# Kernel optimization log

Measured on AMD Instinct MI355X. Metric: run time of the kernel, lower is better.

Reference implementation:

```python
import jax, jax.numpy as jnp
import numpy as np
import math

SIZE = 11
PAD = 5
C1 = 0.01 ** 2
C2 = 0.03 ** 2


def gaussian_window():
    # Matches torch __init__: 1D gaussian (sigma=1.5), normalized, outer product,
    # expanded to depthwise weight of shape (3, 1, 11, 11)
    x = np.arange(SIZE, dtype=np.float32)
    g = np.exp(-((x - SIZE // 2) ** 2) / (2.0 * 1.5 ** 2)).astype(np.float32)
    g = g / g.sum()
    w2d = np.outer(g, g).astype(np.float32)  # (11, 11)
    return jnp.asarray(np.broadcast_to(w2d, (3, 1, SIZE, SIZE)).copy())


def depthwise_conv(x, win):
    return jax.lax.conv_general_dilated(
        x, win,
        window_strides=(1, 1),
        padding=[(PAD, PAD), (PAD, PAD)],
        dimension_numbers=('NCHW', 'OIHW', 'NCHW'),
        feature_group_count=3,
    )


def setup_inputs() -> dict:
    key = jax.random.key(0)
    k1, k2 = jax.random.split(key)
    img1 = jax.random.uniform(k1, (16, 3, 512, 512), dtype=jnp.float32)
    img2 = jax.random.uniform(k2, (16, 3, 512, 512), dtype=jnp.float32)
    return {"img1": img1, "img2": img2, "win": gaussian_window()}


def reference(img1, img2, win):
    mu1 = depthwise_conv(img1, win)
    mu2 = depthwise_conv(img2, win)
    mu1_sq = mu1 * mu1
    mu2_sq = mu2 * mu2
    mu1_mu2 = mu1 * mu2
    sig1_sq = depthwise_conv(img1 * img1, win) - mu1_sq
    sig2_sq = depthwise_conv(img2 * img2, win) - mu2_sq
    sig12 = depthwise_conv(img1 * img2, win) - mu1_mu2
    v = ((2.0 * mu1_mu2 + C1) * (2.0 * sig12 + C2)) / (
        (mu1_sq + mu2_sq + C1) * (sig1_sq + sig2_sq + C2))
    return 1.0 - jnp.mean(v)
```

## Files before the change

### kernel.cpp

```cpp
#include <hip/hip_runtime.h>


#define IMG 512
#define NPIX (16LL * 3 * 512 * 512)
#define GX 8
#define GY 16
#define NBLK (GX * GY * 48)
#define NPART NBLK

typedef short v8s __attribute__((ext_vector_type(8)));
typedef float v4f __attribute__((ext_vector_type(4)));
typedef __bf16 bf2 __attribute__((ext_vector_type(2)));
typedef float f2  __attribute__((ext_vector_type(2)));

static __device__ __forceinline__ int cvtpk2(f2 v) {
    bf2 r = __builtin_convertvector(v, bf2);
    return __builtin_bit_cast(int, r);
}
static __device__ __forceinline__ unsigned f2bf(float f) {
    unsigned u = __float_as_uint(f);
    return (u + 0x7FFFu + ((u >> 16) & 1u)) >> 16;
}

template <bool EDGE>
static __device__ __forceinline__ void load_rt(
    const float* __restrict__ p1, const float* __restrict__ p2,
    int grow, int gcol,
    float4& a0, float4& a1, float4& b0, float4& b1)
{
    if (!EDGE) {
        const float* r1 = p1 + (size_t)grow * IMG + gcol;
        const float* r2 = p2 + (size_t)grow * IMG + gcol;
        a0 = *(const float4*)r1;       a1 = *(const float4*)(r1 + 4);
        b0 = *(const float4*)r2;       b1 = *(const float4*)(r2 + 4);
    } else {
        float4 z4; z4.x = z4.y = z4.z = z4.w = 0.f;
        a0 = a1 = b0 = b1 = z4;
        if ((unsigned)grow < IMG) {
            const float* r1 = p1 + (size_t)grow * IMG;
            const float* r2 = p2 + (size_t)grow * IMG;
            if ((unsigned)gcol < IMG) {
                a0 = *(const float4*)(r1 + gcol);
                b0 = *(const float4*)(r2 + gcol);
            }
            if ((unsigned)(gcol + 4) < IMG) {
                a1 = *(const float4*)(r1 + gcol + 4);
                b1 = *(const float4*)(r2 + gcol + 4);
            }
        }
    }
}

static __device__ __forceinline__ void h_rt(
    float4 a0, float4 a1, float4 b0, float4 b1,
    v8s band, short (*hw)[16][40], int lm, int quad, int slot)
{
    const v4f zacc = {0.f, 0.f, 0.f, 0.f};
    f2 a0l; a0l.x = a0.x; a0l.y = a0.y;   f2 a0h; a0h.x = a0.z; a0h.y = a0.w;
    f2 a1l; a1l.x = a1.x; a1l.y = a1.y;   f2 a1h; a1h.x = a1.z; a1h.y = a1.w;
    f2 b0l; b0l.x = b0.x; b0l.y = b0.y;   f2 b0h; b0h.x = b0.z; b0h.y = b0.w;
    f2 b1l; b1l.x = b1.x; b1l.y = b1.y;   f2 b1h; b1h.x = b1.z; b1h.y = b1.w;

    v8s A[4]; int4 w;
    w.x = cvtpk2(a0l); w.y = cvtpk2(a0h); w.z = cvtpk2(a1l); w.w = cvtpk2(a1h);
    A[0] = __builtin_bit_cast(v8s, w);
    w.x = cvtpk2(b0l); w.y = cvtpk2(b0h); w.z = cvtpk2(b1l); w.w = cvtpk2(b1h);
    A[1] = __builtin_bit_cast(v8s, w);
    w.x = cvtpk2(__builtin_elementwise_fma(a0l, a0l, b0l * b0l));
    w.y = cvtpk2(__builtin_elementwise_fma(a0h, a0h, b0h * b0h));
    w.z = cvtpk2(__builtin_elementwise_fma(a1l, a1l, b1l * b1l));
    w.w = cvtpk2(__builtin_elementwise_fma(a1h, a1h, b1h * b1h));
    A[2] = __builtin_bit_cast(v8s, w);
    w.x = cvtpk2(a0l * b0l); w.y = cvtpk2(a0h * b0h);
    w.z = cvtpk2(a1l * b1l); w.w = cvtpk2(a1h * b1h);
    A[3] = __builtin_bit_cast(v8s, w);

    #pragma unroll
    for (int p = 0; p < 4; ++p) {
        const v4f acc = __builtin_amdgcn_mfma_f32_16x16x32_bf16(A[p], band, zacc, 0, 0, 0);
        int2 w2;
        f2 lo; lo.x = acc[0]; lo.y = acc[1];
        f2 hi; hi.x = acc[2]; hi.y = acc[3];
        w2.x = cvtpk2(lo); w2.y = cvtpk2(hi);
        *(int2*)&hw[p][lm][slot * 16 + quad * 4] = w2;
    }
}

static __device__ __forceinline__ void v_t2(
    v8s band, short (*hw)[16][40], int lm, int quad, int t2, f2& vsum)
{
    const v4f zacc = {0.f, 0.f, 0.f, 0.f};
    const int bs = (quad * 8 + t2 * 16) & 31;
    v4f acc[4];
    #pragma unroll
    for (int p = 0; p < 4; ++p) {
        const v8s hf = *(const v8s*)&hw[p][lm][bs];
        acc[p] = __builtin_amdgcn_mfma_f32_16x16x32_bf16(band, hf, zacc, 0, 0, 0);
    }
    const f2 C1v = {1e-4f, 1e-4f};
    const f2 C2v = {9e-4f, 9e-4f};
    const f2 two = {2.f, 2.f};
    #pragma unroll
    for (int h = 0; h < 2; ++h) {
        f2 m1; m1.x = acc[0][2 * h]; m1.y = acc[0][2 * h + 1];
        f2 m2; m2.x = acc[1][2 * h]; m2.y = acc[1][2 * h + 1];
        f2 es; es.x = acc[2][2 * h]; es.y = acc[2][2 * h + 1];
        f2 ex; ex.x = acc[3][2 * h]; ex.y = acc[3][2 * h + 1];
        const f2 m1s = m1 * m1, m2s = m2 * m2, m12 = m1 * m2;
        const f2 sig = es - m1s - m2s;
        const f2 s12 = ex - m12;
        const f2 num = __builtin_elementwise_fma(two, m12, C1v) *
                       __builtin_elementwise_fma(two, s12, C2v);
        const f2 den = (m1s + m2s + C1v) * (sig + C2v);
        f2 r; r.x = __builtin_amdgcn_rcpf(den.x); r.y = __builtin_amdgcn_rcpf(den.y);
        vsum = __builtin_elementwise_fma(num, r, vsum);
    }
}

__global__ __launch_bounds__(256, 6) void ssim_kernel(
    const float* __restrict__ img1,
    const float* __restrict__ img2,
    const float* __restrict__ win,
    float* __restrict__ partial)
{
    __shared__ __align__(16) short hb[4][4][16][40];

    const int tid  = threadIdx.x;
    const int lane = tid & 63;
    const int wave = tid >> 6;
    const int lm   = lane & 15;
    const int quad = lane >> 4;

    const int bx = blockIdx.x, by = blockIdx.y, z = blockIdx.z;
    const int ty0 = by * 32;

    float gl = 0.f;
    if (lane < 11) gl = win[55 + lane] * rsqrtf(win[60]);
    v8s band;
    #pragma unroll
    for (int j = 0; j < 8; ++j) {
        const int t  = quad * 8 + j - lm - 3;
        const int tc = ((unsigned)t > 10u) ? 11 : t;
        band[j] = (short)f2bf(__shfl(gl, tc));
    }

    const size_t zoff = (size_t)z * IMG * IMG;
    const float* p1 = img1 + zoff;
    const float* p2 = img2 + zoff;

    const int gct = bx * 4 + wave;
    const bool interior = (by > 0) & (by < GY - 1) & (gct > 0) & (gct < 31);
    const int gcol = gct * 16 - 8 + quad * 8;
    short (*hw)[16][40] = hb[wave];

    f2 vsum = {0.f, 0.f};
    {
        float4 a0[2], b0[2], a1[2], b1[2], a2[2], b2[2];
        if (interior) {
            load_rt<false>(p1, p2, ty0 - 8 + 0 * 16 + lm, gcol, a0[0], a0[1], b0[0], b0[1]);
            load_rt<false>(p1, p2, ty0 - 8 + 1 * 16 + lm, gcol, a1[0], a1[1], b1[0], b1[1]);
        } else {
            load_rt<true >(p1, p2, ty0 - 8 + 0 * 16 + lm, gcol, a0[0], a0[1], b0[0], b0[1]);
            load_rt<true >(p1, p2, ty0 - 8 + 1 * 16 + lm, gcol, a1[0], a1[1], b1[0], b1[1]);
        }
        h_rt(a0[0], a0[1], b0[0], b0[1], band, hw, lm, quad, 0);
        h_rt(a1[0], a1[1], b1[0], b1[1], band, hw, lm, quad, 1);
        if (interior)
            load_rt<false>(p1, p2, ty0 - 8 + 2 * 16 + lm, gcol, a2[0], a2[1], b2[0], b2[1]);
        else
            load_rt<true >(p1, p2, ty0 - 8 + 2 * 16 + lm, gcol, a2[0], a2[1], b2[0], b2[1]);
        v_t2(band, hw, lm, quad, 0, vsum);
        h_rt(a2[0], a2[1], b2[0], b2[1], band, hw, lm, quad, 0);
        v_t2(band, hw, lm, quad, 1, vsum);
    }

    float vs = vsum.x + vsum.y;
    #pragma unroll
    for (int off = 32; off > 0; off >>= 1)
        vs += __shfl_down(vs, off, 64);
    if (lane == 0) *(float*)&hb[wave][3][15][36] = vs;
    __syncthreads();
    if (tid == 0) {
        float t = 0.f;
        #pragma unroll
        for (int w = 0; w < 4; ++w) t += *(const float*)&hb[w][3][15][36];
        partial[(z * GY + by) * GX + bx] = t;
    }
}

__global__ __launch_bounds__(512) void finalize_kernel(
    const float* __restrict__ partial, float* __restrict__ out)
{
    __shared__ float red[8];
    const float4* p4 = (const float4*)partial;
    float s = 0.f;
    #pragma unroll
    for (int i = 0; i < NPART / 4 / 512; ++i) {
        const float4 t = p4[i * 512 + threadIdx.x];
        s += (t.x + t.y) + (t.z + t.w);
    }
    #pragma unroll
    for (int off = 32; off > 0; off >>= 1)
        s += __shfl_down(s, off, 64);
    if ((threadIdx.x & 63) == 0) red[threadIdx.x >> 6] = s;
    __syncthreads();
    if (threadIdx.x == 0) {
        float t = 0.f;
        #pragma unroll
        for (int i = 0; i < 8; ++i) t += red[i];
        out[0] = 1.0f - t / (float)NPIX;
    }
}

extern "C" void kernel_launch(void* const* d_in, const int* in_sizes, int n_in,
                              void* d_out, int out_size, void* d_ws, size_t ws_size,
                              hipStream_t stream) {
    const float* img1 = (const float*)d_in[0];
    const float* img2 = (const float*)d_in[1];
    const float* win  = (const float*)d_in[2];
    float* partialb = (float*)d_ws;

    dim3 grid(GX, GY, 48);
    ssim_kernel<<<grid, dim3(256), 0, stream>>>(img1, img2, win, partialb);
    finalize_kernel<<<1, dim3(512), 0, stream>>>(partialb, (float*)d_out);
}
```

Before: 143.8 us.

## Process taller row strips per block with software-pipelined loads to reuse halo rows

Each block now walks 8 row tiles of 16 rows instead of 2, streaming loads for the next tile while running horizontal and vertical MFMA passes on the current one, with sched barriers to keep that order. This cuts redundant halo row loads (from 3 loaded tiles per 2 output tiles to 9 per 8) and the per-block setup such as building the band, at the cost of a 4x smaller grid. Edge handling becomes per-tile rather than per-block, and the finalize kernel is shrunk to match the smaller partial count.

```diff
diff --git a/kernel.cpp b/kernel.cpp
--- a/kernel.cpp
+++ b/kernel.cpp
@@ -4,7 +4,8 @@
 #define IMG 512
 #define NPIX (16LL * 3 * 512 * 512)
 #define GX 8
-#define GY 16
+#define GY 4
+#define NG 8
 #define NBLK (GX * GY * 48)
 #define NPART NBLK
 
@@ -22,40 +23,38 @@
     return (u + 0x7FFFu + ((u >> 16) & 1u)) >> 16;
 }
 
-template <bool EDGE>
-static __device__ __forceinline__ void load_rt(
+static __device__ __forceinline__ void load_g(
     const float* __restrict__ p1, const float* __restrict__ p2,
-    int grow, int gcol,
-    float4& a0, float4& a1, float4& b0, float4& b1)
-{
-    if (!EDGE) {
+    int grow, int gcol, bool edge, float4 (&L)[4])
+{
+    if (!edge) {
         const float* r1 = p1 + (size_t)grow * IMG + gcol;
         const float* r2 = p2 + (size_t)grow * IMG + gcol;
-        a0 = *(const float4*)r1;       a1 = *(const float4*)(r1 + 4);
-        b0 = *(const float4*)r2;       b1 = *(const float4*)(r2 + 4);
+        L[0] = *(const float4*)r1;       L[1] = *(const float4*)(r1 + 4);
+        L[2] = *(const float4*)r2;       L[3] = *(const float4*)(r2 + 4);
     } else {
         float4 z4; z4.x = z4.y = z4.z = z4.w = 0.f;
-        a0 = a1 = b0 = b1 = z4;
+        L[0] = L[1] = L[2] = L[3] = z4;
         if ((unsigned)grow < IMG) {
             const float* r1 = p1 + (size_t)grow * IMG;
             const float* r2 = p2 + (size_t)grow * IMG;
             if ((unsigned)gcol < IMG) {
-                a0 = *(const float4*)(r1 + gcol);
-                b0 = *(const float4*)(r2 + gcol);
+                L[0] = *(const float4*)(r1 + gcol);
+                L[2] = *(const float4*)(r2 + gcol);
             }
             if ((unsigned)(gcol + 4) < IMG) {
-                a1 = *(const float4*)(r1 + gcol + 4);
-                b1 = *(const float4*)(r2 + gcol + 4);
+                L[1] = *(const float4*)(r1 + gcol + 4);
+                L[3] = *(const float4*)(r2 + gcol + 4);
             }
         }
     }
 }
 
 static __device__ __forceinline__ void h_rt(
-    float4 a0, float4 a1, float4 b0, float4 b1,
-    v8s band, short (*hw)[16][40], int lm, int quad, int slot)
+    const float4 (&L)[4], v8s band, short (*hw)[16][40], int lm, int quad, int slot)
 {
     const v4f zacc = {0.f, 0.f, 0.f, 0.f};
+    const float4 a0 = L[0], a1 = L[1], b0 = L[2], b1 = L[3];
     f2 a0l; a0l.x = a0.x; a0l.y = a0.y;   f2 a0h; a0h.x = a0.z; a0h.y = a0.w;
     f2 a1l; a1l.x = a1.x; a1l.y = a1.y;   f2 a1h; a1h.x = a1.z; a1h.y = a1.w;
     f2 b0l; b0l.x = b0.x; b0l.y = b0.y;   f2 b0h; b0h.x = b0.z; b0h.y = b0.w;
@@ -87,10 +86,10 @@
 }
 
 static __device__ __forceinline__ void v_t2(
-    v8s band, short (*hw)[16][40], int lm, int quad, int t2, f2& vsum)
+    v8s band, short (*hw)[16][40], int lm, int quad, int o, f2& vsum)
 {
     const v4f zacc = {0.f, 0.f, 0.f, 0.f};
-    const int bs = (quad * 8 + t2 * 16) & 31;
+    const int bs = (quad * 8 + o * 16) & 31;
     v4f acc[4];
     #pragma unroll
     for (int p = 0; p < 4; ++p) {
@@ -132,7 +131,7 @@
     const int quad = lane >> 4;
 
     const int bx = blockIdx.x, by = blockIdx.y, z = blockIdx.z;
-    const int ty0 = by * 32;
+    const int rowbase = by * (NG * 16);
 
     float gl = 0.f;
     if (lane < 11) gl = win[55 + lane] * rsqrtf(win[60]);
@@ -149,30 +148,36 @@
     const float* p2 = img2 + zoff;
 
     const int gct = bx * 4 + wave;
-    const bool interior = (by > 0) & (by < GY - 1) & (gct > 0) & (gct < 31);
+    const bool colOK = (gct > 0) & (gct < 31);
     const int gcol = gct * 16 - 8 + quad * 8;
     short (*hw)[16][40] = hb[wave];
 
+    const bool topE = (by == 0), botE = (by == GY - 1);
+    #define EDGE_K(k) (!colOK | ((k) == 0 ? topE : false) | ((k) == NG ? botE : false))
+    #define GROW(k)   (rowbase + (k) * 16 - 8 + lm)
+
+    float4 La[4], Lb[4];
     f2 vsum = {0.f, 0.f};
-    {
-        float4 a0[2], b0[2], a1[2], b1[2], a2[2], b2[2];
-        if (interior) {
-            load_rt<false>(p1, p2, ty0 - 8 + 0 * 16 + lm, gcol, a0[0], a0[1], b0[0], b0[1]);
-            load_rt<false>(p1, p2, ty0 - 8 + 1 * 16 + lm, gcol, a1[0], a1[1], b1[0], b1[1]);
-        } else {
-            load_rt<true >(p1, p2, ty0 - 8 + 0 * 16 + lm, gcol, a0[0], a0[1], b0[0], b0[1]);
-            load_rt<true >(p1, p2, ty0 - 8 + 1 * 16 + lm, gcol, a1[0], a1[1], b1[0], b1[1]);
-        }
-        h_rt(a0[0], a0[1], b0[0], b0[1], band, hw, lm, quad, 0);
-        h_rt(a1[0], a1[1], b1[0], b1[1], band, hw, lm, quad, 1);
-        if (interior)
-            load_rt<false>(p1, p2, ty0 - 8 + 2 * 16 + lm, gcol, a2[0], a2[1], b2[0], b2[1]);
-        else
-            load_rt<true >(p1, p2, ty0 - 8 + 2 * 16 + lm, gcol, a2[0], a2[1], b2[0], b2[1]);
-        v_t2(band, hw, lm, quad, 0, vsum);
-        h_rt(a2[0], a2[1], b2[0], b2[1], band, hw, lm, quad, 0);
-        v_t2(band, hw, lm, quad, 1, vsum);
-    }
+
+    load_g(p1, p2, GROW(0), gcol, EDGE_K(0), La);
+    load_g(p1, p2, GROW(1), gcol, EDGE_K(1), Lb);
+    h_rt(La, band, hw, lm, quad, 0);
+
+    #pragma unroll
+    for (int o = 0; o < NG; o += 2) {
+        load_g(p1, p2, GROW(o + 2), gcol, EDGE_K(o + 2), La);
+        __builtin_amdgcn_sched_barrier(0);
+        h_rt(Lb, band, hw, lm, quad, (o + 1) & 1);
+        v_t2(band, hw, lm, quad, o, vsum);
+
+        if (o + 3 <= NG)
+            load_g(p1, p2, GROW(o + 3), gcol, EDGE_K(o + 3), Lb);
+        __builtin_amdgcn_sched_barrier(0);
+        h_rt(La, band, hw, lm, quad, (o + 2) & 1);
+        v_t2(band, hw, lm, quad, o + 1, vsum);
+    }
+    #undef EDGE_K
+    #undef GROW
 
     float vs = vsum.x + vsum.y;
     #pragma unroll
@@ -192,12 +197,10 @@
     const float* __restrict__ partial, float* __restrict__ out)
 {
     __shared__ float red[8];
-    const float4* p4 = (const float4*)partial;
     float s = 0.f;
-    #pragma unroll
-    for (int i = 0; i < NPART / 4 / 512; ++i) {
-        const float4 t = p4[i * 512 + threadIdx.x];
-        s += (t.x + t.y) + (t.z + t.w);
+    if (threadIdx.x < NPART / 4) {
+        const float4 t = ((const float4*)partial)[threadIdx.x];
+        s = (t.x + t.y) + (t.z + t.w);
     }
     #pragma unroll
     for (int off = 32; off > 0; off >>= 1)
```

Result: slower. 202.9 us (+41.1%).
